# Kernel tuning notes

Hardware: AMD Instinct MI355X
Metric: run time of the kernel (lower is better)

The kernel has to match this reference:

```python
import jax, jax.numpy as jnp
import numpy as np

D_MODEL = 1024
NHEAD = 16
D_K = D_MODEL // NHEAD


def setup_inputs() -> dict:
    key = jax.random.key(0)
    ks = jax.random.split(key, 9)
    B, S = 2, 2048
    std = 1.0 / np.sqrt(D_MODEL)
    x = jax.random.normal(ks[0], (B, S, D_MODEL), dtype=jnp.float32)
    Wq = jax.random.uniform(ks[1], (D_MODEL, D_MODEL), jnp.float32, -std, std)
    bq = jax.random.uniform(ks[2], (D_MODEL,), jnp.float32, -std, std)
    Wk = jax.random.uniform(ks[3], (D_MODEL, D_MODEL), jnp.float32, -std, std)
    bk = jax.random.uniform(ks[4], (D_MODEL,), jnp.float32, -std, std)
    Wv = jax.random.uniform(ks[5], (D_MODEL, D_MODEL), jnp.float32, -std, std)
    bv = jax.random.uniform(ks[6], (D_MODEL,), jnp.float32, -std, std)
    Wo = jax.random.uniform(ks[7], (D_MODEL, D_MODEL), jnp.float32, -std, std)
    bo = jax.random.uniform(ks[8], (D_MODEL,), jnp.float32, -std, std)
    return {"x": x, "Wq": Wq, "bq": bq, "Wk": Wk, "bk": bk,
            "Wv": Wv, "bv": bv, "Wo": Wo, "bo": bo}


def reference(x, Wq, bq, Wk, bk, Wv, bv, Wo, bo):
    B, S, _ = x.shape
    scale = jnp.float32(np.sqrt(D_K))
    # Linear layers (torch nn.Linear: y = x @ W.T + b; here W stored as [in,out])
    q = (x @ Wq + bq).reshape(B, S, NHEAD, D_K).transpose(0, 2, 1, 3)  # [B,H,S,Dk]
    k = (x @ Wk + bk).reshape(B, S, NHEAD, D_K).transpose(0, 2, 1, 3)
    v = (x @ Wv + bv).reshape(B, S, NHEAD, D_K).transpose(0, 2, 1, 3)
    scores = jnp.einsum('bhqd,bhkd->bhqk', q, k) / scale  # [B,H,S,S]
    attn = jax.nn.softmax(scores, axis=-1)
    # dropout is identity in eval / deterministic reference
    out = jnp.einsum('bhqk,bhkd->bhqd', attn, v)  # [B,H,S,Dk]
    out = out.transpose(0, 2, 1, 3).reshape(B, S, D_MODEL)
    return out @ Wo + bo
```

## Files before the change

kernel.cpp:

```cpp
#include <hip/hip_runtime.h>
#include <math.h>

#define DM    1024
#define NH    16
#define DK    64
#define SLEN  2048
#define NB    2
#define MROWS (NB*SLEN)
#define QSCALE 0.1803368801111204f

typedef unsigned short u16;
typedef unsigned int   u32;
typedef short  s16x8 __attribute__((ext_vector_type(8)));
typedef __fp16 h16x2 __attribute__((ext_vector_type(2)));
typedef _Float16 f16x8 __attribute__((ext_vector_type(8)));
typedef float  f32x4  __attribute__((ext_vector_type(4)));
typedef float  f32x16 __attribute__((ext_vector_type(16)));

#define MFMA_F16(a,b,c)   __builtin_amdgcn_mfma_f32_16x16x32_f16(a,b,c,0,0,0)
#define MFMA32_F16(a,b,c) __builtin_amdgcn_mfma_f32_32x32x16_f16(a,b,c,0,0,0)

__device__ __forceinline__ void gload16(const void* g, void* l) {
    __builtin_amdgcn_global_load_lds((const __attribute__((address_space(1))) void*)g,
                                     (__attribute__((address_space(3))) void*)l, 16, 0, 0);
}
__device__ __forceinline__ f16x8 as_h(s16x8 v) {
    union { s16x8 s; f16x8 h; } u; u.s = v; return u.h;
}
__device__ __forceinline__ float exp2_hw(float x) {
    float r; asm("v_exp_f32 %0, %1" : "=v"(r) : "v"(x)); return r;
}
__device__ __forceinline__ void pl32swap(u32& a, u32& b) {
    asm volatile("v_permlane32_swap_b32 %0, %1" : "+v"(a), "+v"(b));
}
#define VMCNT0() asm volatile("s_waitcnt vmcnt(0)" ::: "memory")
#define BAR()    __builtin_amdgcn_s_barrier()

__global__ __launch_bounds__(256) void cvt_all(
    const float* __restrict__ x,
    const float* __restrict__ Wq, const float* __restrict__ Wk,
    const float* __restrict__ Wv, const float* __restrict__ Wo,
    _Float16* __restrict__ xh, _Float16* __restrict__ wqkv, _Float16* __restrict__ wo) {
    const int z = blockIdx.z;
    const int t = threadIdx.x;
    if (z == 4) {
        int base = (blockIdx.y * 16 + blockIdx.x) * 256 + t;
#pragma unroll
        for (int u = 0; u < 16; ++u) {
            int i = (base + u * 65536) * 4;
            float4 v = *(const float4*)&x[i];
            float vv[4] = {v.x, v.y, v.z, v.w};
            _Float16 hv[4];
#pragma unroll
            for (int j = 0; j < 4; ++j) hv[j] = (_Float16)vv[j];
            *(ushort4*)&xh[i] = *(ushort4*)hv;
        }
        return;
    }
    __shared__ _Float16 ts[64][72];
    const float* W = (z == 0) ? Wq : (z == 1) ? Wk : (z == 2) ? Wv : Wo;
    _Float16* dst = (z < 3) ? (wqkv + (size_t)z * DM * DM) : wo;
    int k0 = blockIdx.x * 64, n0 = blockIdx.y * 64;
    int kr = t >> 4, c4 = (t & 15) * 4;
#pragma unroll
    for (int u = 0; u < 4; ++u) {
        int k = kr + u * 16;
        float4 v = *(const float4*)&W[(size_t)(k0 + k) * DM + n0 + c4];
        float vv[4] = {v.x, v.y, v.z, v.w};
#pragma unroll
        for (int j = 0; j < 4; ++j) ts[c4 + j][k] = (_Float16)vv[j];
    }
    __syncthreads();
#pragma unroll
    for (int u = 0; u < 4; ++u) {
        int n = kr + u * 16;
        _Float16 hv[4];
#pragma unroll
        for (int j = 0; j < 4; ++j) hv[j] = ts[n][c4 + j];
        *(ushort4*)&dst[(size_t)(n0 + n) * DM + k0 + c4] = *(ushort4*)hv;
    }
}

template<int EPI, int BN_>
__global__ __launch_bounds__(256) void gemm_f16(
    const u16* __restrict__ Ah, const u16* __restrict__ Bt,
    const float* __restrict__ b0, const float* __restrict__ b1, const float* __restrict__ b2,
    float* __restrict__ outf, _Float16* __restrict__ qf,
    _Float16* __restrict__ kfp, _Float16* __restrict__ vtp)
{
    constexpr int NJ = BN_ / 32;
    __shared__ __align__(16) u16 sAh[2][4096];
    __shared__ __align__(16) u16 sB[2][BN_ * 32];
    const int tid = threadIdx.x, wid = tid >> 6, lane = tid & 63;
    const int lq = lane & 15, lk = lane >> 4;
    const int wm = wid >> 1, wn = wid & 1;
    const int bm = blockIdx.x * 128, bn = blockIdx.y * BN_;

    const f32x4 fz = {0.f, 0.f, 0.f, 0.f};
    f32x4 acc[4][NJ];
#pragma unroll
    for (int i = 0; i < 4; ++i)
#pragma unroll
        for (int j = 0; j < NJ; ++j) acc[i][j] = fz;

    auto stage = [&](int b, int k0) {
#pragma unroll
        for (int u = 0; u < 2; ++u) {
            int idx = u * 256 + tid, row = idx >> 2, c = (idx & 3) ^ ((row >> 1) & 3);
            size_t ga = (size_t)(bm + row) * DM + k0 + c * 8;
            gload16(Ah + ga, (char*)&sAh[b][0] + (u * 256 + wid * 64) * 16);
        }
#pragma unroll
        for (int u = 0; u < BN_ / 64; ++u) {
            int idx = u * 256 + tid, row = idx >> 2, c = (idx & 3) ^ ((row >> 1) & 3);
            size_t gb = (size_t)(bn + row) * DM + k0 + c * 8;
            gload16(Bt + gb, (char*)&sB[b][0] + (u * 256 + wid * 64) * 16);
        }
    };
    auto compute = [&](int b) {
        s16x8 avh[4], bv[NJ];
#pragma unroll
        for (int i = 0; i < 4; ++i) {
            int row = wm * 64 + i * 16 + lq;
            int off = row * 32 + ((lk ^ ((row >> 1) & 3)) << 3);
            avh[i] = *(const s16x8*)&sAh[b][off];
        }
#pragma unroll
        for (int j = 0; j < NJ; ++j) {
            int row = wn * (BN_ / 2) + j * 16 + lq;
            int off = row * 32 + ((lk ^ ((row >> 1) & 3)) << 3);
            bv[j] = *(const s16x8*)&sB[b][off];
        }
        __builtin_amdgcn_s_setprio(1);
#pragma unroll
        for (int i = 0; i < 4; ++i)
#pragma unroll
            for (int j = 0; j < NJ; ++j)
                acc[i][j] = MFMA_F16(as_h(avh[i]), as_h(bv[j]), acc[i][j]);
        __builtin_amdgcn_s_setprio(0);
    };

    int buf = 0;
    stage(0, 0);
    VMCNT0(); BAR();
    for (int t = 0; t < 31; ++t) {
        stage(buf ^ 1, (t + 1) * 32);
        compute(buf);
        VMCNT0(); BAR();
        buf ^= 1;
    }
    compute(buf);

#pragma unroll
    for (int j = 0; j < NJ; ++j) {
        int n = bn + wn * (BN_ / 2) + j * 16 + lq;
        if constexpr (EPI == 0) {
            float bias = b0[n];
#pragma unroll
            for (int i = 0; i < 4; ++i)
#pragma unroll
                for (int r = 0; r < 4; ++r) {
                    int m = bm + wm * 64 + i * 16 + lk * 4 + r;
                    outf[(size_t)m * DM + n] = acc[i][j][r] + bias;
                }
        } else {
            int mat = n >> 10, nl = n & 1023;
            int h_ = nl >> 6, d = nl & 63;
            const float* bp = (mat == 0) ? b0 : ((mat == 1) ? b1 : b2);
            float bias = bp[nl];
#pragma unroll
            for (int i = 0; i < 4; ++i) {
                int m0 = bm + wm * 64 + i * 16 + lk * 4;
                int b_ = m0 >> 11, s0 = m0 & (SLEN - 1);
                if (mat == 2) {
                    _Float16 v4[4];
#pragma unroll
                    for (int r = 0; r < 4; ++r) v4[r] = (_Float16)(acc[i][j][r] + bias);
                    *(ushort4*)&vtp[((size_t)(b_ * NH + h_) * DK + d) * SLEN + s0] = *(ushort4*)v4;
                } else {
                    _Float16* dst = (mat == 0) ? qf : kfp;
                    float sc = (mat == 0) ? QSCALE : 1.0f;
#pragma unroll
                    for (int r = 0; r < 4; ++r)
                        dst[((size_t)(b_ * NH + h_) * SLEN + s0 + r) * DK + d] =
                            (_Float16)((acc[i][j][r] + bias) * sc);
                }
            }
        }
    }
}

__global__ __launch_bounds__(128, 2) void attn_mfma(
    const _Float16* __restrict__ qf, const _Float16* __restrict__ kf,
    const _Float16* __restrict__ vt, _Float16* __restrict__ aoh)
{
    __shared__ __align__(16) _Float16 Ks[2][64 * 64], Vs[2][64 * 64];
    const int tid = threadIdx.x, wid = tid >> 6, lane = tid & 63;
    const int ln = lane & 31, l5 = lane >> 5;
    const int phys = blockIdx.x;
    const int virt = (phys & 7) * 128 + (phys >> 3);
    const int bh = virt >> 5, qb = virt & 31;
    const int qrow = qb * 64 + wid * 32 + ln;

    f16x8 qv[4];
#pragma unroll
    for (int t = 0; t < 4; ++t)
        qv[t] = *(const f16x8*)&qf[((size_t)bh * SLEN + qrow) * DK + t * 16 + l5 * 8];

    const _Float16* kbase = kf + (size_t)bh * SLEN * DK;
    const _Float16* vbase = vt + (size_t)bh * DK * SLEN;

    f32x16 O[2];
#pragma unroll
    for (int db = 0; db < 2; ++db)
#pragma unroll
        for (int r = 0; r < 16; ++r) O[db][r] = 0.f;
    float la0 = 0.f, la1 = 0.f, la2 = 0.f, la3 = 0.f;
    const h16x2 ones = {(__fp16)1.0f, (__fp16)1.0f};

    auto stage = [&](int b, int t) {
#pragma unroll
        for (int u = 0; u < 4; ++u) {
            int idx = u * 128 + tid, row = idx >> 3, c = (idx & 7) ^ (row & 7);
            int lo = (u * 128 + wid * 64) * 16;
            gload16(kbase + (size_t)(t * 64 + row) * DK + c * 8, (char*)&Ks[b][0] + lo);
            gload16(vbase + (size_t)row * SLEN + t * 64 + c * 8, (char*)&Vs[b][0] + lo);
        }
    };

    auto compute = [&](int b) {
        f32x16 S[2];
        __builtin_amdgcn_s_setprio(1);
#pragma unroll
        for (int kb = 0; kb < 2; ++kb) {
            f32x16 s;
#pragma unroll
            for (int r = 0; r < 16; ++r) s[r] = 0.f;
            int krow = kb * 32 + ln;
#pragma unroll
            for (int tp = 0; tp < 4; ++tp) {
                int cd = (2 * tp + l5) ^ (krow & 7);
                f16x8 ka = *(const f16x8*)&Ks[b][krow * 64 + cd * 8];
                s = MFMA32_F16(ka, qv[tp], s);
            }
            S[kb] = s;
        }
        __builtin_amdgcn_s_setprio(0);

        u32 pk_[2][8];
#pragma unroll
        for (int kb = 0; kb < 2; ++kb) {
#pragma unroll
            for (int i = 0; i < 8; ++i) {
                float p0 = exp2_hw(S[kb][2 * i]);
                float p1 = exp2_hw(S[kb][2 * i + 1]);
                h16x2 pk = __builtin_amdgcn_cvt_pkrtz(p0, p1);
                switch (i & 3) {
                    case 0: la0 = __builtin_amdgcn_fdot2(pk, ones, la0, false); break;
                    case 1: la1 = __builtin_amdgcn_fdot2(pk, ones, la1, false); break;
                    case 2: la2 = __builtin_amdgcn_fdot2(pk, ones, la2, false); break;
                    default: la3 = __builtin_amdgcn_fdot2(pk, ones, la3, false); break;
                }
                union { h16x2 h; u32 u; } cv; cv.h = pk;
                pk_[kb][i] = cv.u;
            }
            pl32swap(pk_[kb][0], pk_[kb][2]);
            pl32swap(pk_[kb][1], pk_[kb][3]);
            pl32swap(pk_[kb][4], pk_[kb][6]);
            pl32swap(pk_[kb][5], pk_[kb][7]);
        }

        __builtin_amdgcn_s_setprio(1);
#pragma unroll
        for (int kb = 0; kb < 2; ++kb)
#pragma unroll
            for (int t2 = 0; t2 < 2; ++t2) {
                union { u32 w[4]; f16x8 v; } pb;
#pragma unroll
                for (int w = 0; w < 4; ++w) pb.w[w] = pk_[kb][t2 * 4 + w];
#pragma unroll
                for (int db = 0; db < 2; ++db) {
                    int drow = db * 32 + ln;
                    int seg = kb * 2 + t2;
                    int ch = (seg * 2 + l5) ^ (drow & 7);
                    f16x8 va = *(const f16x8*)&Vs[b][drow * 64 + ch * 8];
                    O[db] = MFMA32_F16(va, pb.v, O[db]);
                }
            }
        __builtin_amdgcn_s_setprio(0);
    };

    int buf = 0;
    stage(0, 0);
    VMCNT0(); BAR();
    for (int t = 0; t < SLEN / 64 - 1; ++t) {
        stage(buf ^ 1, t + 1);
        compute(buf);
        VMCNT0(); BAR();
        buf ^= 1;
    }
    compute(buf);

    float lp = (la0 + la1) + (la2 + la3);
    lp += __shfl_xor(lp, 32);
    float inv = 1.0f / lp;
    const int b_ = bh >> 4, h_ = bh & 15;
    size_t rowbase = ((size_t)(b_ * SLEN + qrow)) * DM + h_ * 64;
#pragma unroll
    for (int db = 0; db < 2; ++db)
#pragma unroll
        for (int u = 0; u < 4; ++u) {
            int dbase = 8 * u + 4 * l5 + 32 * db;
            _Float16 h4[4];
#pragma unroll
            for (int j = 0; j < 4; ++j) h4[j] = (_Float16)(O[db][4 * u + j] * inv);
            *(ushort4*)&aoh[rowbase + dbase] = *(ushort4*)h4;
        }
}

extern "C" void kernel_launch(void* const* d_in, const int* in_sizes, int n_in,
                              void* d_out, int out_size, void* d_ws, size_t ws_size,
                              hipStream_t stream) {
    const float* x  = (const float*)d_in[0];
    const float* Wq = (const float*)d_in[1];
    const float* bq = (const float*)d_in[2];
    const float* Wk = (const float*)d_in[3];
    const float* bk = (const float*)d_in[4];
    const float* Wv = (const float*)d_in[5];
    const float* bv = (const float*)d_in[6];
    const float* Wo = (const float*)d_in[7];
    const float* bo = (const float*)d_in[8];
    float* out = (float*)d_out;

    if (ws_size < (size_t)40 * 1024 * 1024) return;
    char* W = (char*)d_ws;
    _Float16* xh   = (_Float16*)(W);
    _Float16* wqkv = (_Float16*)(W + ((size_t)8  << 20));
    _Float16* wo   = (_Float16*)(W + ((size_t)14 << 20));
    _Float16* qf   = (_Float16*)(W + ((size_t)16 << 20));
    _Float16* kf   = (_Float16*)(W + ((size_t)24 << 20));
    _Float16* vt   = (_Float16*)(W + ((size_t)32 << 20));
    _Float16* aoh  = xh;

    cvt_all<<<dim3(16, 16, 5), dim3(256), 0, stream>>>(
        x, Wq, Wk, Wv, Wo, xh, wqkv, wo);

    gemm_f16<1, 64><<<dim3(32, 48), dim3(256), 0, stream>>>(
        (const u16*)xh, (const u16*)wqkv,
        bq, bk, bv, nullptr, qf, kf, vt);

    attn_mfma<<<dim3(1024), dim3(128), 0, stream>>>(qf, kf, vt, aoh);

    gemm_f16<0, 64><<<dim3(32, 16), dim3(256), 0, stream>>>(
        (const u16*)aoh, (const u16*)wo,
        bo, nullptr, nullptr, out, nullptr, nullptr, nullptr);
}
```

Before: 135.1 us.

## Restructure attention into single-wave blocks handling two query tiles, barrier-free

Attention now runs one 64-thread wave per block. Each wave processes two 32-row query tiles that share every K/V fragment read from LDS, and it walks the key sequence in 32-key steps with new LDS swizzle layouts. Because a block is a single wave, the workgroup barriers are removed; only vmcnt waits remain. The QKV projection GEMM also moves to a wider 128 tile with half the grid. The costs are higher register pressure, since each wave now holds four output accumulators, and twice as many loop iterations with smaller loads.

```diff
diff --git a/kernel.cpp b/kernel.cpp
--- a/kernel.cpp
+++ b/kernel.cpp
@@ -190,132 +190,136 @@
     }
 }
 
-__global__ __launch_bounds__(128, 2) void attn_mfma(
+__global__ __launch_bounds__(64) void attn_pw(
     const _Float16* __restrict__ qf, const _Float16* __restrict__ kf,
     const _Float16* __restrict__ vt, _Float16* __restrict__ aoh)
 {
-    __shared__ __align__(16) _Float16 Ks[2][64 * 64], Vs[2][64 * 64];
-    const int tid = threadIdx.x, wid = tid >> 6, lane = tid & 63;
+    __shared__ __align__(16) _Float16 Ks[2][32 * 64];
+    __shared__ __align__(16) _Float16 Vs[2][32 * 64];
+    const int lane = threadIdx.x;
     const int ln = lane & 31, l5 = lane >> 5;
     const int phys = blockIdx.x;
     const int virt = (phys & 7) * 128 + (phys >> 3);
-    const int bh = virt >> 5, qb = virt & 31;
-    const int qrow = qb * 64 + wid * 32 + ln;
-
-    f16x8 qv[4];
-#pragma unroll
-    for (int t = 0; t < 4; ++t)
-        qv[t] = *(const f16x8*)&qf[((size_t)bh * SLEN + qrow) * DK + t * 16 + l5 * 8];
+    const int bh = virt >> 5, qw = virt & 31;
+    const int qrow0 = qw * 64 + ln;
+    const int qrow1 = qrow0 + 32;
+
+    f16x8 qv0[4], qv1[4];
+#pragma unroll
+    for (int tp = 0; tp < 4; ++tp) {
+        qv0[tp] = *(const f16x8*)&qf[((size_t)bh * SLEN + qrow0) * DK + tp * 16 + l5 * 8];
+        qv1[tp] = *(const f16x8*)&qf[((size_t)bh * SLEN + qrow1) * DK + tp * 16 + l5 * 8];
+    }
 
     const _Float16* kbase = kf + (size_t)bh * SLEN * DK;
     const _Float16* vbase = vt + (size_t)bh * DK * SLEN;
 
-    f32x16 O[2];
+    int koff[4], voff[4];
+#pragma unroll
+    for (int u = 0; u < 4; ++u) {
+        int idx = u * 64 + lane;
+        int krow = idx >> 3, kch = lane & 7, kg = kch ^ (krow & 7);
+        koff[u] = krow * DK + kg * 8;
+        int j = idx >> 3, h = (lane & 7) >> 2, vch = lane & 3, vg = vch ^ (j & 3);
+        voff[u] = (2 * j + h) * SLEN + vg * 8;
+    }
+
+    f32x16 O0[2], O1[2];
 #pragma unroll
     for (int db = 0; db < 2; ++db)
 #pragma unroll
-        for (int r = 0; r < 16; ++r) O[db][r] = 0.f;
-    float la0 = 0.f, la1 = 0.f, la2 = 0.f, la3 = 0.f;
+        for (int r = 0; r < 16; ++r) { O0[db][r] = 0.f; O1[db][r] = 0.f; }
+    float la[2][2] = {{0.f, 0.f}, {0.f, 0.f}};
     const h16x2 ones = {(__fp16)1.0f, (__fp16)1.0f};
 
     auto stage = [&](int b, int t) {
 #pragma unroll
-        for (int u = 0; u < 4; ++u) {
-            int idx = u * 128 + tid, row = idx >> 3, c = (idx & 7) ^ (row & 7);
-            int lo = (u * 128 + wid * 64) * 16;
-            gload16(kbase + (size_t)(t * 64 + row) * DK + c * 8, (char*)&Ks[b][0] + lo);
-            gload16(vbase + (size_t)row * SLEN + t * 64 + c * 8, (char*)&Vs[b][0] + lo);
-        }
+        for (int u = 0; u < 4; ++u)
+            gload16(kbase + (size_t)t * 32 * DK + koff[u], (char*)&Ks[b][0] + u * 1024);
+#pragma unroll
+        for (int u = 0; u < 4; ++u)
+            gload16(vbase + (size_t)t * 32 + voff[u], (char*)&Vs[b][0] + u * 1024);
     };
 
     auto compute = [&](int b) {
-        f32x16 S[2];
+        f32x16 S0, S1;
+#pragma unroll
+        for (int r = 0; r < 16; ++r) { S0[r] = 0.f; S1[r] = 0.f; }
         __builtin_amdgcn_s_setprio(1);
 #pragma unroll
-        for (int kb = 0; kb < 2; ++kb) {
-            f32x16 s;
-#pragma unroll
-            for (int r = 0; r < 16; ++r) s[r] = 0.f;
-            int krow = kb * 32 + ln;
-#pragma unroll
-            for (int tp = 0; tp < 4; ++tp) {
-                int cd = (2 * tp + l5) ^ (krow & 7);
-                f16x8 ka = *(const f16x8*)&Ks[b][krow * 64 + cd * 8];
-                s = MFMA32_F16(ka, qv[tp], s);
+        for (int tp = 0; tp < 4; ++tp) {
+            f16x8 ka = *(const f16x8*)&Ks[b][ln * 64 + (((2 * tp + l5) ^ (ln & 7)) << 3)];
+            S0 = MFMA32_F16(ka, qv0[tp], S0);
+            S1 = MFMA32_F16(ka, qv1[tp], S1);
+        }
+        __builtin_amdgcn_s_setprio(0);
+
+        u32 pk0[8], pk1[8];
+#pragma unroll
+        for (int i = 0; i < 8; ++i) {
+            float a0 = exp2_hw(S0[2 * i]), a1 = exp2_hw(S0[2 * i + 1]);
+            h16x2 pa = __builtin_amdgcn_cvt_pkrtz(a0, a1);
+            la[0][i & 1] = __builtin_amdgcn_fdot2(pa, ones, la[0][i & 1], false);
+            union { h16x2 h; u32 u; } ca; ca.h = pa; pk0[i] = ca.u;
+            float b0_ = exp2_hw(S1[2 * i]), b1_ = exp2_hw(S1[2 * i + 1]);
+            h16x2 pb = __builtin_amdgcn_cvt_pkrtz(b0_, b1_);
+            la[1][i & 1] = __builtin_amdgcn_fdot2(pb, ones, la[1][i & 1], false);
+            union { h16x2 h; u32 u; } cb; cb.h = pb; pk1[i] = cb.u;
+        }
+        pl32swap(pk0[0], pk0[2]); pl32swap(pk0[1], pk0[3]);
+        pl32swap(pk0[4], pk0[6]); pl32swap(pk0[5], pk0[7]);
+        pl32swap(pk1[0], pk1[2]); pl32swap(pk1[1], pk1[3]);
+        pl32swap(pk1[4], pk1[6]); pl32swap(pk1[5], pk1[7]);
+
+        __builtin_amdgcn_s_setprio(1);
+#pragma unroll
+        for (int t2 = 0; t2 < 2; ++t2) {
+            union { u32 w[4]; f16x8 v; } p0, p1;
+#pragma unroll
+            for (int w = 0; w < 4; ++w) { p0.w[w] = pk0[t2 * 4 + w]; p1.w[w] = pk1[t2 * 4 + w]; }
+#pragma unroll
+            for (int db = 0; db < 2; ++db) {
+                int drow = db * 32 + ln;
+                int j = drow >> 1, h = drow & 1;
+                int ch = (t2 * 2 + l5) ^ (j & 3);
+                f16x8 va = *(const f16x8*)&Vs[b][j * 64 + h * 32 + ch * 8];
+                O0[db] = MFMA32_F16(va, p0.v, O0[db]);
+                O1[db] = MFMA32_F16(va, p1.v, O1[db]);
             }
-            S[kb] = s;
-        }
-        __builtin_amdgcn_s_setprio(0);
-
-        u32 pk_[2][8];
-#pragma unroll
-        for (int kb = 0; kb < 2; ++kb) {
-#pragma unroll
-            for (int i = 0; i < 8; ++i) {
-                float p0 = exp2_hw(S[kb][2 * i]);
-                float p1 = exp2_hw(S[kb][2 * i + 1]);
-                h16x2 pk = __builtin_amdgcn_cvt_pkrtz(p0, p1);
-                switch (i & 3) {
-                    case 0: la0 = __builtin_amdgcn_fdot2(pk, ones, la0, false); break;
-                    case 1: la1 = __builtin_amdgcn_fdot2(pk, ones, la1, false); break;
-                    case 2: la2 = __builtin_amdgcn_fdot2(pk, ones, la2, false); break;
-                    default: la3 = __builtin_amdgcn_fdot2(pk, ones, la3, false); break;
-                }
-                union { h16x2 h; u32 u; } cv; cv.h = pk;
-                pk_[kb][i] = cv.u;
-            }
-            pl32swap(pk_[kb][0], pk_[kb][2]);
-            pl32swap(pk_[kb][1], pk_[kb][3]);
-            pl32swap(pk_[kb][4], pk_[kb][6]);
-            pl32swap(pk_[kb][5], pk_[kb][7]);
-        }
-
-        __builtin_amdgcn_s_setprio(1);
-#pragma unroll
-        for (int kb = 0; kb < 2; ++kb)
-#pragma unroll
-            for (int t2 = 0; t2 < 2; ++t2) {
-                union { u32 w[4]; f16x8 v; } pb;
-#pragma unroll
-                for (int w = 0; w < 4; ++w) pb.w[w] = pk_[kb][t2 * 4 + w];
-#pragma unroll
-                for (int db = 0; db < 2; ++db) {
-                    int drow = db * 32 + ln;
-                    int seg = kb * 2 + t2;
-                    int ch = (seg * 2 + l5) ^ (drow & 7);
-                    f16x8 va = *(const f16x8*)&Vs[b][drow * 64 + ch * 8];
-                    O[db] = MFMA32_F16(va, pb.v, O[db]);
-                }
-            }
+        }
         __builtin_amdgcn_s_setprio(0);
     };
 
     int buf = 0;
     stage(0, 0);
-    VMCNT0(); BAR();
-    for (int t = 0; t < SLEN / 64 - 1; ++t) {
-        stage(buf ^ 1, t + 1);
+    VMCNT0();
+    for (int t = 0; t < SLEN / 32; ++t) {
+        if (t + 1 < SLEN / 32) stage(buf ^ 1, t + 1);
         compute(buf);
-        VMCNT0(); BAR();
+        VMCNT0();
         buf ^= 1;
     }
-    compute(buf);
-
-    float lp = (la0 + la1) + (la2 + la3);
-    lp += __shfl_xor(lp, 32);
-    float inv = 1.0f / lp;
+
     const int b_ = bh >> 4, h_ = bh & 15;
-    size_t rowbase = ((size_t)(b_ * SLEN + qrow)) * DM + h_ * 64;
-#pragma unroll
-    for (int db = 0; db < 2; ++db)
-#pragma unroll
-        for (int u = 0; u < 4; ++u) {
-            int dbase = 8 * u + 4 * l5 + 32 * db;
-            _Float16 h4[4];
-#pragma unroll
-            for (int j = 0; j < 4; ++j) h4[j] = (_Float16)(O[db][4 * u + j] * inv);
-            *(ushort4*)&aoh[rowbase + dbase] = *(ushort4*)h4;
-        }
+#pragma unroll
+    for (int g = 0; g < 2; ++g) {
+        float lp = la[g][0] + la[g][1];
+        lp += __shfl_xor(lp, 32);
+        float inv = 1.0f / lp;
+        int qrow = (g == 0) ? qrow0 : qrow1;
+        size_t rowbase = ((size_t)(b_ * SLEN + qrow)) * DM + h_ * 64;
+        const f32x16* Og = (g == 0) ? O0 : O1;
+#pragma unroll
+        for (int db = 0; db < 2; ++db)
+#pragma unroll
+            for (int u = 0; u < 4; ++u) {
+                int dbase = 8 * u + 4 * l5 + 32 * db;
+                _Float16 h4[4];
+#pragma unroll
+                for (int j = 0; j < 4; ++j) h4[j] = (_Float16)(Og[db][4 * u + j] * inv);
+                *(ushort4*)&aoh[rowbase + dbase] = *(ushort4*)h4;
+            }
+    }
 }
 
 extern "C" void kernel_launch(void* const* d_in, const int* in_sizes, int n_in,
@@ -345,11 +349,11 @@
     cvt_all<<<dim3(16, 16, 5), dim3(256), 0, stream>>>(
         x, Wq, Wk, Wv, Wo, xh, wqkv, wo);
 
-    gemm_f16<1, 64><<<dim3(32, 48), dim3(256), 0, stream>>>(
+    gemm_f16<1, 128><<<dim3(32, 24), dim3(256), 0, stream>>>(
         (const u16*)xh, (const u16*)wqkv,
         bq, bk, bv, nullptr, qf, kf, vt);
 
-    attn_mfma<<<dim3(1024), dim3(128), 0, stream>>>(qf, kf, vt, aoh);
+    attn_pw<<<dim3(1024), dim3(64), 0, stream>>>(qf, kf, vt, aoh);
 
     gemm_f16<0, 64><<<dim3(32, 16), dim3(256), 0, stream>>>(
         (const u16*)aoh, (const u16*)wo,
```

Result: no change. 136.8 us (+1.3%).

## Split attention over KV halves with merge kernel, enlarge GEMM tiles

Applied to the files above, without the earlier changes.

Attention blocks now process 128 query rows across 4 waves over half of the key/value sequence. Each writes unnormalized fp16 partial outputs and row sums, and a new merge kernel combines and normalizes them. The QKV projection GEMM uses 128x128 tiles and the output GEMM uses a 64-wide K step with its own kernel. The intent is better K/V reuse and GEMM efficiency, at the cost of an extra kernel, extra partial-output traffic and fp16 storage of unnormalized partials.

```diff
diff --git a/kernel.cpp b/kernel.cpp
--- a/kernel.cpp
+++ b/kernel.cpp
@@ -81,44 +81,38 @@
     }
 }
 
-template<int EPI, int BN_>
-__global__ __launch_bounds__(256) void gemm_f16(
+__global__ __launch_bounds__(256) void gemm_qkv(
     const u16* __restrict__ Ah, const u16* __restrict__ Bt,
     const float* __restrict__ b0, const float* __restrict__ b1, const float* __restrict__ b2,
-    float* __restrict__ outf, _Float16* __restrict__ qf,
-    _Float16* __restrict__ kfp, _Float16* __restrict__ vtp)
+    _Float16* __restrict__ qf, _Float16* __restrict__ kfp, _Float16* __restrict__ vtp)
 {
-    constexpr int NJ = BN_ / 32;
     __shared__ __align__(16) u16 sAh[2][4096];
-    __shared__ __align__(16) u16 sB[2][BN_ * 32];
+    __shared__ __align__(16) u16 sB[2][4096];
     const int tid = threadIdx.x, wid = tid >> 6, lane = tid & 63;
     const int lq = lane & 15, lk = lane >> 4;
     const int wm = wid >> 1, wn = wid & 1;
-    const int bm = blockIdx.x * 128, bn = blockIdx.y * BN_;
+    const int bm = blockIdx.x * 128, bn = blockIdx.y * 128;
 
     const f32x4 fz = {0.f, 0.f, 0.f, 0.f};
-    f32x4 acc[4][NJ];
+    f32x4 acc[4][4];
 #pragma unroll
     for (int i = 0; i < 4; ++i)
 #pragma unroll
-        for (int j = 0; j < NJ; ++j) acc[i][j] = fz;
+        for (int j = 0; j < 4; ++j) acc[i][j] = fz;
 
     auto stage = [&](int b, int k0) {
 #pragma unroll
         for (int u = 0; u < 2; ++u) {
             int idx = u * 256 + tid, row = idx >> 2, c = (idx & 3) ^ ((row >> 1) & 3);
             size_t ga = (size_t)(bm + row) * DM + k0 + c * 8;
-            gload16(Ah + ga, (char*)&sAh[b][0] + (u * 256 + wid * 64) * 16);
-        }
-#pragma unroll
-        for (int u = 0; u < BN_ / 64; ++u) {
-            int idx = u * 256 + tid, row = idx >> 2, c = (idx & 3) ^ ((row >> 1) & 3);
             size_t gb = (size_t)(bn + row) * DM + k0 + c * 8;
-            gload16(Bt + gb, (char*)&sB[b][0] + (u * 256 + wid * 64) * 16);
+            int lo = (u * 256 + wid * 64) * 16;
+            gload16(Ah + ga, (char*)&sAh[b][0] + lo);
+            gload16(Bt + gb, (char*)&sB[b][0] + lo);
         }
     };
     auto compute = [&](int b) {
-        s16x8 avh[4], bv[NJ];
+        s16x8 avh[4], bv[4];
 #pragma unroll
         for (int i = 0; i < 4; ++i) {
             int row = wm * 64 + i * 16 + lq;
@@ -126,8 +120,8 @@
             avh[i] = *(const s16x8*)&sAh[b][off];
         }
 #pragma unroll
-        for (int j = 0; j < NJ; ++j) {
-            int row = wn * (BN_ / 2) + j * 16 + lq;
+        for (int j = 0; j < 4; ++j) {
+            int row = wn * 64 + j * 16 + lq;
             int off = row * 32 + ((lk ^ ((row >> 1) & 3)) << 3);
             bv[j] = *(const s16x8*)&sB[b][off];
         }
@@ -135,7 +129,7 @@
 #pragma unroll
         for (int i = 0; i < 4; ++i)
 #pragma unroll
-            for (int j = 0; j < NJ; ++j)
+            for (int j = 0; j < 4; ++j)
                 acc[i][j] = MFMA_F16(as_h(avh[i]), as_h(bv[j]), acc[i][j]);
         __builtin_amdgcn_s_setprio(0);
     };
@@ -152,63 +146,137 @@
     compute(buf);
 
 #pragma unroll
-    for (int j = 0; j < NJ; ++j) {
-        int n = bn + wn * (BN_ / 2) + j * 16 + lq;
-        if constexpr (EPI == 0) {
-            float bias = b0[n];
+    for (int j = 0; j < 4; ++j) {
+        int n = bn + wn * 64 + j * 16 + lq;
+        int mat = n >> 10, nl = n & 1023;
+        int h_ = nl >> 6, d = nl & 63;
+        const float* bp = (mat == 0) ? b0 : ((mat == 1) ? b1 : b2);
+        float bias = bp[nl];
+#pragma unroll
+        for (int i = 0; i < 4; ++i) {
+            int m0 = bm + wm * 64 + i * 16 + lk * 4;
+            int b_ = m0 >> 11, s0 = m0 & (SLEN - 1);
+            if (mat == 2) {
+                _Float16 v4[4];
+#pragma unroll
+                for (int r = 0; r < 4; ++r) v4[r] = (_Float16)(acc[i][j][r] + bias);
+                *(ushort4*)&vtp[((size_t)(b_ * NH + h_) * DK + d) * SLEN + s0] = *(ushort4*)v4;
+            } else {
+                _Float16* dst = (mat == 0) ? qf : kfp;
+                float sc = (mat == 0) ? QSCALE : 1.0f;
+#pragma unroll
+                for (int r = 0; r < 4; ++r)
+                    dst[((size_t)(b_ * NH + h_) * SLEN + s0 + r) * DK + d] =
+                        (_Float16)((acc[i][j][r] + bias) * sc);
+            }
+        }
+    }
+}
+
+__global__ __launch_bounds__(256) void gemm_out(
+    const u16* __restrict__ Ah, const u16* __restrict__ Bt,
+    const float* __restrict__ b0, float* __restrict__ outf)
+{
+    __shared__ __align__(16) u16 sA[2][128 * 64];
+    __shared__ __align__(16) u16 sB[2][64 * 64];
+    const int tid = threadIdx.x, wid = tid >> 6, lane = tid & 63;
+    const int lq = lane & 15, lk = lane >> 4;
+    const int wm = wid >> 1, wn = wid & 1;
+    const int bm = blockIdx.x * 128, bn = blockIdx.y * 64;
+
+    const f32x4 fz = {0.f, 0.f, 0.f, 0.f};
+    f32x4 acc[4][2];
+#pragma unroll
+    for (int i = 0; i < 4; ++i)
+#pragma unroll
+        for (int j = 0; j < 2; ++j) acc[i][j] = fz;
+
+    auto stage = [&](int b, int k0) {
+#pragma unroll
+        for (int u = 0; u < 4; ++u) {
+            int idx = u * 256 + tid, row = idx >> 3, c = (idx & 7) ^ (row & 7);
+            gload16(Ah + (size_t)(bm + row) * DM + k0 + c * 8,
+                    (char*)&sA[b][0] + (u * 256 + wid * 64) * 16);
+        }
+#pragma unroll
+        for (int u = 0; u < 2; ++u) {
+            int idx = u * 256 + tid, row = idx >> 3, c = (idx & 7) ^ (row & 7);
+            gload16(Bt + (size_t)(bn + row) * DM + k0 + c * 8,
+                    (char*)&sB[b][0] + (u * 256 + wid * 64) * 16);
+        }
+    };
+    auto compute = [&](int b) {
+        __builtin_amdgcn_s_setprio(1);
+#pragma unroll
+        for (int kk = 0; kk < 2; ++kk) {
+            s16x8 av[4], bv[2];
+#pragma unroll
+            for (int i = 0; i < 4; ++i) {
+                int row = wm * 64 + i * 16 + lq;
+                av[i] = *(const s16x8*)&sA[b][row * 64 + (((kk * 4 + lk) ^ (row & 7)) << 3)];
+            }
+#pragma unroll
+            for (int j = 0; j < 2; ++j) {
+                int row = wn * 32 + j * 16 + lq;
+                bv[j] = *(const s16x8*)&sB[b][row * 64 + (((kk * 4 + lk) ^ (row & 7)) << 3)];
+            }
 #pragma unroll
             for (int i = 0; i < 4; ++i)
 #pragma unroll
-                for (int r = 0; r < 4; ++r) {
-                    int m = bm + wm * 64 + i * 16 + lk * 4 + r;
-                    outf[(size_t)m * DM + n] = acc[i][j][r] + bias;
-                }
-        } else {
-            int mat = n >> 10, nl = n & 1023;
-            int h_ = nl >> 6, d = nl & 63;
-            const float* bp = (mat == 0) ? b0 : ((mat == 1) ? b1 : b2);
-            float bias = bp[nl];
-#pragma unroll
-            for (int i = 0; i < 4; ++i) {
-                int m0 = bm + wm * 64 + i * 16 + lk * 4;
-                int b_ = m0 >> 11, s0 = m0 & (SLEN - 1);
-                if (mat == 2) {
-                    _Float16 v4[4];
-#pragma unroll
-                    for (int r = 0; r < 4; ++r) v4[r] = (_Float16)(acc[i][j][r] + bias);
-                    *(ushort4*)&vtp[((size_t)(b_ * NH + h_) * DK + d) * SLEN + s0] = *(ushort4*)v4;
-                } else {
-                    _Float16* dst = (mat == 0) ? qf : kfp;
-                    float sc = (mat == 0) ? QSCALE : 1.0f;
-#pragma unroll
-                    for (int r = 0; r < 4; ++r)
-                        dst[((size_t)(b_ * NH + h_) * SLEN + s0 + r) * DK + d] =
-                            (_Float16)((acc[i][j][r] + bias) * sc);
-                }
-            }
-        }
-    }
-}
-
-__global__ __launch_bounds__(128, 2) void attn_mfma(
+                for (int j = 0; j < 2; ++j)
+                    acc[i][j] = MFMA_F16(as_h(av[i]), as_h(bv[j]), acc[i][j]);
+        }
+        __builtin_amdgcn_s_setprio(0);
+    };
+
+    int buf = 0;
+    stage(0, 0);
+    VMCNT0(); BAR();
+    for (int t = 0; t < 15; ++t) {
+        stage(buf ^ 1, (t + 1) * 64);
+        compute(buf);
+        VMCNT0(); BAR();
+        buf ^= 1;
+    }
+    compute(buf);
+
+#pragma unroll
+    for (int j = 0; j < 2; ++j) {
+        int n = bn + wn * 32 + j * 16 + lq;
+        float bias = b0[n];
+#pragma unroll
+        for (int i = 0; i < 4; ++i)
+#pragma unroll
+            for (int r = 0; r < 4; ++r) {
+                int m = bm + wm * 64 + i * 16 + lk * 4 + r;
+                outf[(size_t)m * DM + n] = acc[i][j][r] + bias;
+            }
+    }
+}
+
+__global__ __launch_bounds__(256, 4) void attn_part(
     const _Float16* __restrict__ qf, const _Float16* __restrict__ kf,
-    const _Float16* __restrict__ vt, _Float16* __restrict__ aoh)
+    const _Float16* __restrict__ vt,
+    _Float16* __restrict__ opart, float* __restrict__ lpart)
 {
     __shared__ __align__(16) _Float16 Ks[2][64 * 64], Vs[2][64 * 64];
     const int tid = threadIdx.x, wid = tid >> 6, lane = tid & 63;
     const int ln = lane & 31, l5 = lane >> 5;
     const int phys = blockIdx.x;
     const int virt = (phys & 7) * 128 + (phys >> 3);
-    const int bh = virt >> 5, qb = virt & 31;
-    const int qrow = qb * 64 + wid * 32 + ln;
+    const int bh = virt >> 5, rem = virt & 31;
+    const int qb = rem >> 1, half = rem & 1;
+    const int qrow = qb * 128 + wid * 32 + ln;
+    const int kv0 = half * (SLEN / 2);
+    const int NT = (SLEN / 2) / 64;
 
     f16x8 qv[4];
 #pragma unroll
-    for (int t = 0; t < 4; ++t)
-        qv[t] = *(const f16x8*)&qf[((size_t)bh * SLEN + qrow) * DK + t * 16 + l5 * 8];
-
-    const _Float16* kbase = kf + (size_t)bh * SLEN * DK;
-    const _Float16* vbase = vt + (size_t)bh * DK * SLEN;
+    for (int tp = 0; tp < 4; ++tp)
+        qv[tp] = *(const f16x8*)&qf[((size_t)bh * SLEN + qrow) * DK + tp * 16 + l5 * 8];
+
+    const _Float16* kbase = kf + (size_t)bh * SLEN * DK + (size_t)kv0 * DK;
+    const _Float16* vbase = vt + (size_t)bh * DK * SLEN + kv0;
 
     f32x16 O[2];
 #pragma unroll
@@ -220,9 +288,9 @@
 
     auto stage = [&](int b, int t) {
 #pragma unroll
-        for (int u = 0; u < 4; ++u) {
-            int idx = u * 128 + tid, row = idx >> 3, c = (idx & 7) ^ (row & 7);
-            int lo = (u * 128 + wid * 64) * 16;
+        for (int u = 0; u < 2; ++u) {
+            int idx = u * 256 + tid, row = idx >> 3, c = (idx & 7) ^ (row & 7);
+            int lo = (u * 256 + wid * 64) * 16;
             gload16(kbase + (size_t)(t * 64 + row) * DK + c * 8, (char*)&Ks[b][0] + lo);
             gload16(vbase + (size_t)row * SLEN + t * 64 + c * 8, (char*)&Vs[b][0] + lo);
         }
@@ -293,7 +361,7 @@
     int buf = 0;
     stage(0, 0);
     VMCNT0(); BAR();
-    for (int t = 0; t < SLEN / 64 - 1; ++t) {
+    for (int t = 0; t < NT - 1; ++t) {
         stage(buf ^ 1, t + 1);
         compute(buf);
         VMCNT0(); BAR();
@@ -303,9 +371,10 @@
 
     float lp = (la0 + la1) + (la2 + la3);
     lp += __shfl_xor(lp, 32);
-    float inv = 1.0f / lp;
     const int b_ = bh >> 4, h_ = bh & 15;
-    size_t rowbase = ((size_t)(b_ * SLEN + qrow)) * DM + h_ * 64;
+    const int grow = b_ * SLEN + qrow;
+    if (l5 == 0) lpart[((size_t)half * 4096 + grow) * NH + h_] = lp;
+    size_t rowbase = ((size_t)half * 4096 + grow) * DM + h_ * 64;
 #pragma unroll
     for (int db = 0; db < 2; ++db)
 #pragma unroll
@@ -313,9 +382,26 @@
             int dbase = 8 * u + 4 * l5 + 32 * db;
             _Float16 h4[4];
 #pragma unroll
-            for (int j = 0; j < 4; ++j) h4[j] = (_Float16)(O[db][4 * u + j] * inv);
-            *(ushort4*)&aoh[rowbase + dbase] = *(ushort4*)h4;
-        }
+            for (int j = 0; j < 4; ++j) h4[j] = (_Float16)(O[db][4 * u + j]);
+            *(ushort4*)&opart[rowbase + dbase] = *(ushort4*)h4;
+        }
+}
+
+__global__ __launch_bounds__(256) void attn_merge(
+    const _Float16* __restrict__ opart, const float* __restrict__ lpart,
+    _Float16* __restrict__ aoh)
+{
+    int idx = blockIdx.x * 256 + threadIdx.x;
+    int row = idx >> 7, cq = idx & 127;
+    int col = cq * 8, h = col >> 6;
+    float l = lpart[(size_t)row * NH + h] + lpart[((size_t)4096 + row) * NH + h];
+    float inv = 1.0f / l;
+    f16x8 a = *(const f16x8*)&opart[(size_t)row * DM + col];
+    f16x8 b = *(const f16x8*)&opart[(size_t)(4096 + row) * DM + col];
+    f16x8 o;
+#pragma unroll
+    for (int j = 0; j < 8; ++j) o[j] = (_Float16)(((float)a[j] + (float)b[j]) * inv);
+    *(f16x8*)&aoh[(size_t)row * DM + col] = o;
 }
 
 extern "C" void kernel_launch(void* const* d_in, const int* in_sizes, int n_in,
@@ -332,26 +418,28 @@
     const float* bo = (const float*)d_in[8];
     float* out = (float*)d_out;
 
-    if (ws_size < (size_t)40 * 1024 * 1024) return;
+    if (ws_size < (size_t)58 * 1024 * 1024) return;
     char* W = (char*)d_ws;
-    _Float16* xh   = (_Float16*)(W);
-    _Float16* wqkv = (_Float16*)(W + ((size_t)8  << 20));
-    _Float16* wo   = (_Float16*)(W + ((size_t)14 << 20));
-    _Float16* qf   = (_Float16*)(W + ((size_t)16 << 20));
-    _Float16* kf   = (_Float16*)(W + ((size_t)24 << 20));
-    _Float16* vt   = (_Float16*)(W + ((size_t)32 << 20));
-    _Float16* aoh  = xh;
+    _Float16* xh    = (_Float16*)(W);
+    _Float16* wqkv  = (_Float16*)(W + ((size_t)8  << 20));
+    _Float16* wo    = (_Float16*)(W + ((size_t)14 << 20));
+    _Float16* qf    = (_Float16*)(W + ((size_t)16 << 20));
+    _Float16* kf    = (_Float16*)(W + ((size_t)24 << 20));
+    _Float16* vt    = (_Float16*)(W + ((size_t)32 << 20));
+    _Float16* opart = (_Float16*)(W + ((size_t)40 << 20));
+    float*    lpart = (float*)(W + ((size_t)57 << 20));
+    _Float16* aoh   = xh;
 
     cvt_all<<<dim3(16, 16, 5), dim3(256), 0, stream>>>(
         x, Wq, Wk, Wv, Wo, xh, wqkv, wo);
 
-    gemm_f16<1, 64><<<dim3(32, 48), dim3(256), 0, stream>>>(
-        (const u16*)xh, (const u16*)wqkv,
-        bq, bk, bv, nullptr, qf, kf, vt);
-
-    attn_mfma<<<dim3(1024), dim3(128), 0, stream>>>(qf, kf, vt, aoh);
-
-    gemm_f16<0, 64><<<dim3(32, 16), dim3(256), 0, stream>>>(
-        (const u16*)aoh, (const u16*)wo,
-        bo, nullptr, nullptr, out, nullptr, nullptr, nullptr);
-}
+    gemm_qkv<<<dim3(32, 24), dim3(256), 0, stream>>>(
+        (const u16*)xh, (const u16*)wqkv, bq, bk, bv, qf, kf, vt);
+
+    attn_part<<<dim3(1024), dim3(256), 0, stream>>>(qf, kf, vt, opart, lpart);
+
+    attn_merge<<<dim3(2048), dim3(256), 0, stream>>>(opart, lpart, aoh);
+
+    gemm_out<<<dim3(32, 16), dim3(256), 0, stream>>>(
+        (const u16*)aoh, (const u16*)wo, bo, out);
+}
```

After: 119.0 us. -11.9%, faster.
